# Optimization experiments

Measured on AMD Instinct MI355X. Metric: run time of the kernel, lower is better.

The kernel has to match this reference:

```python
import jax, jax.numpy as jnp
import numpy as np

N = 50000      # nodes
E = 600000     # edges
D_IN = 128
HID = 128
D_OUT = 3
G = 32         # graphs in the batch


def setup_inputs() -> dict:
    key = jax.random.key(0)
    ks = jax.random.split(key, 16)
    s = 0.05
    x = jax.random.normal(ks[0], (N, D_IN), dtype=jnp.float32)
    edge_index = jax.random.randint(ks[1], (2, E), 0, N, dtype=jnp.int64)
    batch = jnp.sort(jax.random.randint(ks[2], (N,), 0, G, dtype=jnp.int64))
    return {
        "x": x,
        "conv0_Wl": jax.random.normal(ks[3], (HID, D_IN), jnp.float32) * s,
        "conv0_bl": jnp.zeros((HID,), jnp.float32),
        "conv0_Wr": jax.random.normal(ks[4], (HID, D_IN), jnp.float32) * s,
        "lin1_W": jax.random.normal(ks[5], (HID, HID), jnp.float32) * s,
        "lin1_b": jnp.zeros((HID,), jnp.float32),
        "conv1_Wl": jax.random.normal(ks[6], (HID, HID), jnp.float32) * s,
        "conv1_bl": jnp.zeros((HID,), jnp.float32),
        "conv1_Wr": jax.random.normal(ks[7], (HID, HID), jnp.float32) * s,
        "fc_W": jax.random.normal(ks[8], (D_OUT, HID), jnp.float32) * s,
        "fc_b": jnp.zeros((D_OUT,), jnp.float32),
        "edge_index": edge_index,
        "batch": batch,
    }


def _sage_conv(x, Wl, bl, Wr, src, dst):
    # PyG SAGEConv (mean aggr): out = lin_l(mean_{j in N(i)} x_j) + lin_r(x_i)
    msg = x[src]                                              # [E, d] gather
    ssum = jax.ops.segment_sum(msg, dst, num_segments=N)      # [N, d]
    cnt = jax.ops.segment_sum(jnp.ones((src.shape[0],), x.dtype), dst, num_segments=N)
    aggr = ssum / jnp.maximum(cnt, 1.0)[:, None]
    return aggr @ Wl.T + bl + x @ Wr.T


def reference(x, conv0_Wl, conv0_bl, conv0_Wr, lin1_W, lin1_b,
              conv1_Wl, conv1_bl, conv1_Wr, fc_W, fc_b,
              edge_index, batch):
    src, dst = edge_index[0], edge_index[1]
    # conv0 -> relu (dropout is identity in eval mode)
    h = jax.nn.relu(_sage_conv(x, conv0_Wl, conv0_bl, conv0_Wr, src, dst))
    # Linear -> relu -> SAGEConv -> relu
    h = jax.nn.relu(h @ lin1_W.T + lin1_b)
    h = jax.nn.relu(_sage_conv(h, conv1_Wl, conv1_bl, conv1_Wr, src, dst))
    # global_mean_pool over graphs
    gsum = jax.ops.segment_sum(h, batch, num_segments=G)
    gcnt = jax.ops.segment_sum(jnp.ones((h.shape[0],), h.dtype), batch, num_segments=G)
    pooled = gsum / jnp.maximum(gcnt, 1.0)[:, None]           # [G, HID]
    return pooled @ fc_W.T + fc_b                             # [G, D_OUT]
```

## Files before the change

kernel.cpp:

```cpp
#include <hip/hip_runtime.h>
#include <hip/hip_bf16.h>
#include <stdint.h>


typedef __attribute__((ext_vector_type(8))) short short8;
typedef __attribute__((ext_vector_type(4))) float f32x4;
typedef __attribute__((ext_vector_type(2))) float f32x2;

__device__ __forceinline__ float bits2f(uint32_t b) {
    union { uint32_t u; float f; } c; c.u = b; return c.f;
}
__device__ __forceinline__ unsigned short f2bf(float f) {
    __hip_bfloat16 h = __float2bfloat16(f);
    union { __hip_bfloat16 h; unsigned short u; } c; c.h = h; return c.u;
}
__device__ __forceinline__ uint32_t pack2bf(float a, float b) {
    return (uint32_t)f2bf(a) | ((uint32_t)f2bf(b) << 16);
}
__device__ __forceinline__ uint32_t pk4fp8(float f0, float f1, float f2, float f3) {
    int o = 0;
    o = __builtin_amdgcn_cvt_pk_fp8_f32(f0, f1, o, false);
    o = __builtin_amdgcn_cvt_pk_fp8_f32(f2, f3, o, true);
    return (uint32_t)o;
}
__device__ __forceinline__ void acc8f8(float* a, uint2 v) {
    f32x2 p0 = __builtin_amdgcn_cvt_pk_f32_fp8((int)v.x, false);
    f32x2 p1 = __builtin_amdgcn_cvt_pk_f32_fp8((int)v.x, true);
    f32x2 p2 = __builtin_amdgcn_cvt_pk_f32_fp8((int)v.y, false);
    f32x2 p3 = __builtin_amdgcn_cvt_pk_f32_fp8((int)v.y, true);
    a[0] += p0.x; a[1] += p0.y; a[2] += p1.x; a[3] += p1.y;
    a[4] += p2.x; a[5] += p2.y; a[6] += p3.x; a[7] += p3.y;
}

__device__ __forceinline__ void detect_flags(const unsigned short* x,
                                             const int* ei,
                                             int& isbf, int& is64) {
    int lane = threadIdx.x & 63;
    unsigned short h = x[lane];
    int e = (h >> 7) & 0xFF;
    unsigned long long mbf = __ballot(e >= 102 && e <= 137);
    unsigned long long m64 = __ballot(ei[2 * lane + 1] != 0);
    isbf = (__popcll(mbf) >= 52) ? 1 : 0;
    is64 = (m64 == 0ULL) ? 1 : 0;
}

#define WB_W0L 0
#define WB_W0R 16384
#define WB_W1  32768
#define WB_W1L 49152
#define WB_W1R 65536
#define WB_TOTAL 81920
#define CF_B0L 0
#define CF_B1  128
#define CF_B1L 256
#define CF_FCW 384
#define CF_FCB 768
#define CF_TOTAL 771

__global__ __launch_bounds__(256) void prep_kernel(
    const void* x, const int* __restrict__ ei,
    const void* s0, const void* s1, const void* s2, const void* s3,
    const void* s4, const void* f0, const void* f1, const void* f2,
    const void* f3, const void* f4,
    unsigned short* __restrict__ Hb, uint2* __restrict__ Xf8,
    unsigned short* __restrict__ wb,
    float* __restrict__ cf, int* __restrict__ cnt, int* __restrict__ nbr,
    int* __restrict__ flags, int n8, int E, int EG, int WC) {
    int isbf, is64;
    detect_flags((const unsigned short*)x, ei, isbf, is64);
    int b = blockIdx.x;
    if (b == 0 && threadIdx.x == 0) { flags[0] = isbf; flags[1] = is64; }

    if (b < EG) {
        int e = b * 256 + threadIdx.x;
        if (e >= E) return;
        int s, d;
        if (is64) { s = ei[2 * e]; d = ei[2 * (E + e)]; }
        else      { s = ei[e];     d = ei[E + e]; }
        int pos = atomicAdd(&cnt[d], 1);
        if (pos < 64) nbr[((size_t)d << 6) + pos] = s;
    } else if (b < EG + WC) {
        int i = (b - EG) * 256 + threadIdx.x;
        if (i < WB_TOTAL) {
            const void* p; int k = i & 16383;
            switch (i >> 14) {
                case 0: p = s0; break;
                case 1: p = s1; break;
                case 2: p = s2; break;
                case 3: p = s3; break;
                default: p = s4; break;
            }
            wb[i] = isbf ? ((const unsigned short*)p)[k]
                         : f2bf(((const float*)p)[k]);
        } else {
            int j = i - WB_TOTAL;
            if (j >= CF_TOTAL) return;
            const void* p; int k;
            if      (j < CF_B1)  { p = f0; k = j; }
            else if (j < CF_B1L) { p = f1; k = j - CF_B1; }
            else if (j < CF_FCW) { p = f2; k = j - CF_B1L; }
            else if (j < CF_FCB) { p = f3; k = j - CF_FCW; }
            else                 { p = f4; k = j - CF_FCB; }
            cf[j] = isbf ? bits2f((uint32_t)((const unsigned short*)p)[k] << 16)
                         : ((const float*)p)[k];
        }
    } else {
        int i = (b - EG - WC) * 256 + threadIdx.x;
        if (i >= n8) return;
        float f[8];
        if (isbf) {
            uint4 d = ((const uint4*)x)[i];
            f[0] = bits2f(d.x << 16); f[1] = bits2f(d.x & 0xffff0000u);
            f[2] = bits2f(d.y << 16); f[3] = bits2f(d.y & 0xffff0000u);
            f[4] = bits2f(d.z << 16); f[5] = bits2f(d.z & 0xffff0000u);
            f[6] = bits2f(d.w << 16); f[7] = bits2f(d.w & 0xffff0000u);
        } else {
            float4 a = ((const float4*)x)[2 * i];
            float4 c = ((const float4*)x)[2 * i + 1];
            f[0] = a.x; f[1] = a.y; f[2] = a.z; f[3] = a.w;
            f[4] = c.x; f[5] = c.y; f[6] = c.z; f[7] = c.w;
            uint4 d;
            d.x = pack2bf(f[0], f[1]); d.y = pack2bf(f[2], f[3]);
            d.z = pack2bf(f[4], f[5]); d.w = pack2bf(f[6], f[7]);
            ((uint4*)Hb)[i] = d;
        }
        uint2 o8;
        o8.x = pk4fp8(f[0], f[1], f[2], f[3]);
        o8.y = pk4fp8(f[4], f[5], f[6], f[7]);
        Xf8[i] = o8;
    }
}

template <bool LIN1, bool POOL>
__device__ __forceinline__ void conv_core(
    const void* xsel, const unsigned short* __restrict__ Hbuf,
    const uint2* __restrict__ G8,
    const int* __restrict__ cnt, const int* __restrict__ nbr,
    const unsigned short* __restrict__ Wl, const unsigned short* __restrict__ Wr,
    const float* __restrict__ bias,
    const unsigned short* __restrict__ W2, const float* __restrict__ bias2,
    unsigned short* __restrict__ Hdst, uint2* __restrict__ Hdst8,
    float* __restrict__ pool, const int* __restrict__ batch,
    const int* __restrict__ flags, int N) {
    __shared__ unsigned short bufA[16 * 136];
    __shared__ unsigned short bufB[LIN1 ? 16 * 136 : 1];
    __shared__ float pbuf[POOL ? 512 : 1];
    const int t = threadIdx.x;
    const int lane = t & 63;
    const int w = t >> 6;
    const int l15 = lane & 15;
    const int kq = lane >> 4;
    const int m0 = blockIdx.x * 16;

    const int flags0 = flags[0];
    const unsigned short* Hs = flags0 ? (const unsigned short*)xsel : Hbuf;

    int f64 = 0, gmin = 0, g[4];
    if (POOL) {
        f64 = flags[1];
        gmin = f64 ? batch[2 * m0] : batch[m0];
#pragma unroll
        for (int r = 0; r < 4; r++) {
            int gr = m0 + kq * 4 + r;
            g[r] = (gr < N) ? (f64 ? batch[2 * gr] : batch[gr]) : -1;
        }
        for (int i = t; i < 512; i += 256) pbuf[i] = 0.f;
    }

    short8 xf[4];
    {
        int xr = m0 + l15; if (xr >= N) xr = N - 1;
        const unsigned short* xrow = Hs + (size_t)xr * 128 + kq * 8;
#pragma unroll
        for (int kc = 0; kc < 4; kc++) xf[kc] = *(const short8*)(xrow + kc * 32);
    }
    float bc[2];
    const int nt0 = w * 2;
    bc[0] = bias[nt0 * 16 + l15];
    bc[1] = bias[(nt0 + 1) * 16 + l15];

    {
        const int row = w * 4 + kq;
        const int node = m0 + row;
        float a[8] = {0.f, 0.f, 0.f, 0.f, 0.f, 0.f, 0.f, 0.f};
        float invd = 0.f;
        if (node < N) {
            int dcnt = cnt[node];
            invd = 1.f / fmaxf((float)dcnt, 1.f);
            if (dcnt > 64) dcnt = 64;
            const int* nrow = nbr + ((size_t)node << 6);
            for (int base = 0; base < dcnt; base += 16) {
                int c = dcnt - base; if (c > 16) c = 16;
                int idx = (l15 < c) ? nrow[base + l15] : 0;
                int it = 0;
                for (; it + 4 <= c; it += 4) {
                    int j0 = __shfl(idx, kq * 16 + it, 64);
                    int j1 = __shfl(idx, kq * 16 + it + 1, 64);
                    int j2 = __shfl(idx, kq * 16 + it + 2, 64);
                    int j3 = __shfl(idx, kq * 16 + it + 3, 64);
                    uint2 v0 = G8[(size_t)j0 * 16 + l15];
                    uint2 v1 = G8[(size_t)j1 * 16 + l15];
                    uint2 v2 = G8[(size_t)j2 * 16 + l15];
                    uint2 v3 = G8[(size_t)j3 * 16 + l15];
                    acc8f8(a, v0); acc8f8(a, v1); acc8f8(a, v2); acc8f8(a, v3);
                }
                for (; it < c; ++it) {
                    int j = __shfl(idx, kq * 16 + it, 64);
                    acc8f8(a, G8[(size_t)j * 16 + l15]);
                }
            }
        }
        uint4 o;
        o.x = pack2bf(a[0] * invd, a[1] * invd);
        o.y = pack2bf(a[2] * invd, a[3] * invd);
        o.z = pack2bf(a[4] * invd, a[5] * invd);
        o.w = pack2bf(a[6] * invd, a[7] * invd);
        *(uint4*)(bufA + row * 136 + l15 * 8) = o;
    }
    __syncthreads();

    short8 af[4];
#pragma unroll
    for (int kc = 0; kc < 4; kc++)
        af[kc] = *(const short8*)(bufA + l15 * 136 + kc * 32 + kq * 8);

    f32x4 acc[2];
    acc[0] = (f32x4){0.f, 0.f, 0.f, 0.f};
    acc[1] = (f32x4){0.f, 0.f, 0.f, 0.f};
#pragma unroll
    for (int kc = 0; kc < 4; kc++) {
#pragma unroll
        for (int u = 0; u < 2; u++) {
            const size_t woff = (size_t)((nt0 + u) * 16 + l15) * 128 + kc * 32 + kq * 8;
            acc[u] = __builtin_amdgcn_mfma_f32_16x16x32_bf16(
                xf[kc], *(const short8*)(Wr + woff), acc[u], 0, 0, 0);
            acc[u] = __builtin_amdgcn_mfma_f32_16x16x32_bf16(
                af[kc], *(const short8*)(Wl + woff), acc[u], 0, 0, 0);
        }
    }

    if (LIN1) {
#pragma unroll
        for (int u = 0; u < 2; u++) {
#pragma unroll
            for (int r = 0; r < 4; r++) {
                bufB[(kq * 4 + r) * 136 + (nt0 + u) * 16 + l15] =
                    f2bf(fmaxf(acc[u][r] + bc[u], 0.f));
            }
        }
        __syncthreads();
        short8 hf[4];
#pragma unroll
        for (int kc = 0; kc < 4; kc++)
            hf[kc] = *(const short8*)(bufB + l15 * 136 + kc * 32 + kq * 8);
        acc[0] = (f32x4){0.f, 0.f, 0.f, 0.f};
        acc[1] = (f32x4){0.f, 0.f, 0.f, 0.f};
        bc[0] = bias2[nt0 * 16 + l15];
        bc[1] = bias2[(nt0 + 1) * 16 + l15];
#pragma unroll
        for (int kc = 0; kc < 4; kc++) {
#pragma unroll
            for (int u = 0; u < 2; u++) {
                const size_t woff = (size_t)((nt0 + u) * 16 + l15) * 128 + kc * 32 + kq * 8;
                acc[u] = __builtin_amdgcn_mfma_f32_16x16x32_bf16(
                    hf[kc], *(const short8*)(W2 + woff), acc[u], 0, 0, 0);
            }
        }
    }

    if (POOL) {
        bool same = (g[0] == g[1]) && (g[1] == g[2]) && (g[2] == g[3]) && (g[0] >= 0);
#pragma unroll
        for (int u = 0; u < 2; u++) {
            int c = (nt0 + u) * 16 + l15;
            float v0 = fmaxf(acc[u][0] + bc[u], 0.f);
            float v1 = fmaxf(acc[u][1] + bc[u], 0.f);
            float v2 = fmaxf(acc[u][2] + bc[u], 0.f);
            float v3 = fmaxf(acc[u][3] + bc[u], 0.f);
            if (same) {
                int si = g[0] - gmin;
                float s4 = (v0 + v1) + (v2 + v3);
                if (si < 4) atomicAdd(&pbuf[si * 128 + c], s4);
                else        atomicAdd(&pool[g[0] * 128 + c], s4);
            } else {
                float vr[4] = {v0, v1, v2, v3};
#pragma unroll
                for (int r = 0; r < 4; r++) {
                    if (g[r] >= 0) {
                        int si = g[r] - gmin;
                        if (si < 4) atomicAdd(&pbuf[si * 128 + c], vr[r]);
                        else        atomicAdd(&pool[g[r] * 128 + c], vr[r]);
                    }
                }
            }
        }
        __syncthreads();
        for (int i = t; i < 512; i += 256) {
            float v = pbuf[i];
            if (v != 0.f)
                atomicAdd(&pool[(gmin + (i >> 7)) * 128 + (i & 127)], v);
        }
    } else {
#pragma unroll
        for (int u = 0; u < 2; u++) {
#pragma unroll
            for (int r = 0; r < 4; r++) {
                bufA[(kq * 4 + r) * 136 + (nt0 + u) * 16 + l15] =
                    f2bf(fmaxf(acc[u][r] + bc[u], 0.f));
            }
        }
        __syncthreads();
        int row = t >> 4, colsh = (t & 15) * 8;
        uint4 val = *(const uint4*)(bufA + row * 136 + colsh);
        if (m0 + row < N) {
            *(uint4*)(Hdst + (size_t)(m0 + row) * 128 + colsh) = val;
            float h0 = bits2f(val.x << 16), h1 = bits2f(val.x & 0xffff0000u);
            float h2 = bits2f(val.y << 16), h3 = bits2f(val.y & 0xffff0000u);
            float h4 = bits2f(val.z << 16), h5 = bits2f(val.z & 0xffff0000u);
            float h6 = bits2f(val.w << 16), h7 = bits2f(val.w & 0xffff0000u);
            uint2 e8;
            e8.x = pk4fp8(h0, h1, h2, h3);
            e8.y = pk4fp8(h4, h5, h6, h7);
            Hdst8[(size_t)(m0 + row) * 16 + (colsh >> 3)] = e8;
        }
    }
}

__global__ __launch_bounds__(256) void conv01_kernel(
    const void* xsel, const unsigned short* __restrict__ Hbuf,
    const uint2* __restrict__ G8,
    const int* __restrict__ cnt, const int* __restrict__ nbr,
    const unsigned short* __restrict__ Wl, const unsigned short* __restrict__ Wr,
    const float* __restrict__ bias,
    const unsigned short* __restrict__ W2, const float* __restrict__ bias2,
    unsigned short* __restrict__ Hdst, uint2* __restrict__ Hdst8,
    const int* __restrict__ flags, int N) {
    conv_core<true, false>(xsel, Hbuf, G8, cnt, nbr, Wl, Wr, bias, W2, bias2,
                           Hdst, Hdst8, nullptr, nullptr, flags, N);
}

__global__ __launch_bounds__(256) void conv1p_kernel(
    const unsigned short* __restrict__ Hbuf, const uint2* __restrict__ G8,
    const int* __restrict__ cnt, const int* __restrict__ nbr,
    const unsigned short* __restrict__ Wl, const unsigned short* __restrict__ Wr,
    const float* __restrict__ bias,
    float* __restrict__ pool, const int* __restrict__ batch,
    const int* __restrict__ flags, int N) {
    conv_core<false, true>(Hbuf, Hbuf, G8, cnt, nbr, Wl, Wr, bias,
                           nullptr, nullptr, nullptr, nullptr, pool, batch,
                           flags, N);
}

__global__ void fc_kernel(const float* __restrict__ pool,
                          const int* __restrict__ batch,
                          const float* __restrict__ W,
                          const float* __restrict__ b,
                          void* __restrict__ out,
                          const int* __restrict__ flags, int N, int G) {
    __shared__ int gst[64];
    int t = threadIdx.x;
    int f64 = flags[1];
    int isbf = flags[0];
    if (t <= G) {
        int lo = 0, hi = N;
        while (lo < hi) {
            int mid = (lo + hi) >> 1;
            int bv = f64 ? batch[2 * mid] : batch[mid];
            if (bv < t) lo = mid + 1; else hi = mid;
        }
        gst[t] = lo;
    }
    __syncthreads();
    if (t >= G * 3) return;
    int g = t / 3, o = t % 3;
    int cnt = gst[g + 1] - gst[g];
    float inv = 1.f / fmaxf((float)cnt, 1.f);
    float acc = 0.f;
    for (int k = 0; k < 128; k++)
        acc += pool[g * 128 + k] * W[o * 128 + k];
    float r = acc * inv + b[o];
    if (isbf) ((__hip_bfloat16*)out)[t] = __float2bfloat16(r);
    else      ((float*)out)[t] = r;
}

extern "C" void kernel_launch(void* const* d_in, const int* in_sizes, int n_in,
                              void* d_out, int out_size, void* d_ws, size_t ws_size,
                              hipStream_t stream) {
    const void* x   = d_in[0];
    const void* W0l = d_in[1];
    const void* b0l = d_in[2];
    const void* W0r = d_in[3];
    const void* W1  = d_in[4];
    const void* b1  = d_in[5];
    const void* W1l = d_in[6];
    const void* b1l = d_in[7];
    const void* W1r = d_in[8];
    const void* fcW = d_in[9];
    const void* fcb = d_in[10];
    const int* edge_index = (const int*)d_in[11];
    const int* batch      = (const int*)d_in[12];

    const int N = in_sizes[12];
    const int E = in_sizes[11] / 2;
    const int G = out_size / 3;

    char* ws = (char*)d_ws;
    auto align64 = [](size_t v) { return (v + 63) & ~(size_t)63; };
    size_t off = 0;
    size_t OFF_CNT  = off; off = align64(off + (size_t)N * 4);
    size_t OFF_POOL = off; off = align64(off + (size_t)G * 128 * 4);
    size_t MEMSET_BYTES = off;
    size_t OFF_FLAGS = off; off = align64(off + 64);
    size_t OFF_NBR  = off; off = align64(off + (size_t)N * 64 * 4);
    size_t OFF_WB   = off; off = align64(off + (size_t)WB_TOTAL * 2);
    size_t OFF_CF   = off; off = align64(off + (size_t)CF_TOTAL * 4);
    size_t OFF_XF8  = off; off = align64(off + (size_t)N * 128);
    size_t OFF_H2F8 = off; off = align64(off + (size_t)N * 128);
    size_t OFF_HB   = off; off = align64(off + ((size_t)N + 64) * 128 * 2);
    size_t OFF_H2   = off; off = align64(off + ((size_t)N + 64) * 128 * 2);
    (void)ws_size;

    int*    cnt    = (int*)(ws + OFF_CNT);
    float*  pool   = (float*)(ws + OFF_POOL);
    int*    flags  = (int*)(ws + OFF_FLAGS);
    int*    nbr    = (int*)(ws + OFF_NBR);
    unsigned short* wb = (unsigned short*)(ws + OFF_WB);
    float*  cf     = (float*)(ws + OFF_CF);
    uint2*  Xf8    = (uint2*)(ws + OFF_XF8);
    uint2*  H2f8   = (uint2*)(ws + OFF_H2F8);
    unsigned short* Hb = (unsigned short*)(ws + OFF_HB);
    unsigned short* H2 = (unsigned short*)(ws + OFF_H2);

    hipMemsetAsync(ws, 0, MEMSET_BYTES, stream);

    int n8 = (N * 128) / 8;
    int EG  = (E + 255) / 256;
    int WC  = (WB_TOTAL + CF_TOTAL + 255) / 256;
    int CVT = (n8 + 255) / 256;
    prep_kernel<<<EG + WC + CVT, 256, 0, stream>>>(
        x, edge_index, W0l, W0r, W1, W1l, W1r, b0l, b1, b1l, fcW, fcb,
        Hb, Xf8, wb, cf, cnt, nbr, flags, n8, E, EG, WC);

    int cgrid = (N + 15) / 16;

    conv01_kernel<<<cgrid, 256, 0, stream>>>(
        x, Hb, Xf8, cnt, nbr, wb + WB_W0L, wb + WB_W0R, cf + CF_B0L,
        wb + WB_W1, cf + CF_B1, H2, H2f8, flags, N);

    conv1p_kernel<<<cgrid, 256, 0, stream>>>(
        H2, H2f8, cnt, nbr, wb + WB_W1L, wb + WB_W1R, cf + CF_B1L,
        pool, batch, flags, N);

    fc_kernel<<<1, 128, 0, stream>>>(pool, batch, cf + CF_FCW, cf + CF_FCB,
                                     d_out, flags, N, G);

    (void)in_sizes; (void)n_in; (void)out_size;
}
```

Baseline: 240.9 us.

## Use persistent blocks with atomic tile counter and batched neighbor gathers

Turns the two conv kernels into persistent kernels capped at 2048 blocks that pull 16-row tiles from a global atomic counter. The next tile index is prefetched into shared memory with double buffering. The first 32 neighbor indices are preloaded and gathered in unrolled chunks of eight loads to raise memory-level parallelism. This is meant to cut block launch overhead and gather latency, at the cost of an extra atomic and barrier per tile and wasted zero-padded loads for low-degree nodes.

```diff
diff --git a/kernel.cpp b/kernel.cpp
--- a/kernel.cpp
+++ b/kernel.cpp
@@ -141,188 +141,234 @@
     const unsigned short* __restrict__ W2, const float* __restrict__ bias2,
     unsigned short* __restrict__ Hdst, uint2* __restrict__ Hdst8,
     float* __restrict__ pool, const int* __restrict__ batch,
-    const int* __restrict__ flags, int N) {
+    const int* __restrict__ flags, int* ctr, int N) {
     __shared__ unsigned short bufA[16 * 136];
     __shared__ unsigned short bufB[LIN1 ? 16 * 136 : 1];
     __shared__ float pbuf[POOL ? 512 : 1];
+    __shared__ int s_next[2];
     const int t = threadIdx.x;
     const int lane = t & 63;
     const int w = t >> 6;
     const int l15 = lane & 15;
     const int kq = lane >> 4;
-    const int m0 = blockIdx.x * 16;
+    const int nt0 = w * 2;
+    const int ntiles = (N + 15) >> 4;
 
     const int flags0 = flags[0];
     const unsigned short* Hs = flags0 ? (const unsigned short*)xsel : Hbuf;
-
-    int f64 = 0, gmin = 0, g[4];
-    if (POOL) {
-        f64 = flags[1];
-        gmin = f64 ? batch[2 * m0] : batch[m0];
-#pragma unroll
-        for (int r = 0; r < 4; r++) {
-            int gr = m0 + kq * 4 + r;
-            g[r] = (gr < N) ? (f64 ? batch[2 * gr] : batch[gr]) : -1;
-        }
-        for (int i = t; i < 512; i += 256) pbuf[i] = 0.f;
+    const int f64 = POOL ? flags[1] : 0;
+
+    const float b0a = bias[nt0 * 16 + l15];
+    const float b0b = bias[(nt0 + 1) * 16 + l15];
+    float b2a = 0.f, b2b = 0.f;
+    if (LIN1) {
+        b2a = bias2[nt0 * 16 + l15];
+        b2b = bias2[(nt0 + 1) * 16 + l15];
     }
 
-    short8 xf[4];
-    {
-        int xr = m0 + l15; if (xr >= N) xr = N - 1;
-        const unsigned short* xrow = Hs + (size_t)xr * 128 + kq * 8;
-#pragma unroll
-        for (int kc = 0; kc < 4; kc++) xf[kc] = *(const short8*)(xrow + kc * 32);
-    }
-    float bc[2];
-    const int nt0 = w * 2;
-    bc[0] = bias[nt0 * 16 + l15];
-    bc[1] = bias[(nt0 + 1) * 16 + l15];
-
-    {
+    if (t == 0) s_next[0] = atomicAdd(ctr, 1);
+    __syncthreads();
+    int tile = s_next[0];
+    int par = 1;
+
+    while (tile < ntiles) {
+        if (t == 0) s_next[par] = atomicAdd(ctr, 1);
+        const int m0 = tile * 16;
+
+        int gmin = 0, g[4];
+        if (POOL) {
+            gmin = f64 ? batch[2 * m0] : batch[m0];
+#pragma unroll
+            for (int r = 0; r < 4; r++) {
+                int gr = m0 + kq * 4 + r;
+                g[r] = (gr < N) ? (f64 ? batch[2 * gr] : batch[gr]) : -1;
+            }
+            for (int i = t; i < 512; i += 256) pbuf[i] = 0.f;
+        }
+
         const int row = w * 4 + kq;
         const int node = m0 + row;
-        float a[8] = {0.f, 0.f, 0.f, 0.f, 0.f, 0.f, 0.f, 0.f};
+        int c = 0;
         float invd = 0.f;
+        const int* nrow = nbr;
+        int i0 = 0, i1 = 0;
         if (node < N) {
             int dcnt = cnt[node];
             invd = 1.f / fmaxf((float)dcnt, 1.f);
-            if (dcnt > 64) dcnt = 64;
-            const int* nrow = nbr + ((size_t)node << 6);
-            for (int base = 0; base < dcnt; base += 16) {
-                int c = dcnt - base; if (c > 16) c = 16;
-                int idx = (l15 < c) ? nrow[base + l15] : 0;
+            c = dcnt > 64 ? 64 : dcnt;
+            nrow = nbr + ((size_t)node << 6);
+            i0 = (l15 < c) ? nrow[l15] : 0;
+            i1 = (16 + l15 < c) ? nrow[16 + l15] : 0;
+        }
+
+        short8 xf[4];
+        {
+            int xr = m0 + l15; if (xr >= N) xr = N - 1;
+            const unsigned short* xrow = Hs + (size_t)xr * 128 + kq * 8;
+#pragma unroll
+            for (int kc = 0; kc < 4; kc++) xf[kc] = *(const short8*)(xrow + kc * 32);
+        }
+
+        {
+            float a[8] = {0.f, 0.f, 0.f, 0.f, 0.f, 0.f, 0.f, 0.f};
+            int nch = (c + 7) >> 3; if (nch > 4) nch = 4;
+#pragma unroll
+            for (int ch = 0; ch < 4; ++ch) {
+                if (ch < nch) {
+                    uint2 vv[8];
+#pragma unroll
+                    for (int u = 0; u < 8; ++u) {
+                        const int s = ch * 8 + u;
+                        int jv = __shfl((s < 16) ? i0 : i1, kq * 16 + (s & 15), 64);
+                        int j = (s < c) ? jv : 0;
+                        vv[u] = G8[(size_t)j * 16 + l15];
+                        if (s >= c) { vv[u].x = 0u; vv[u].y = 0u; }
+                    }
+#pragma unroll
+                    for (int u = 0; u < 8; ++u) acc8f8(a, vv[u]);
+                }
+            }
+            for (int base = 32; base < c; base += 16) {
+                int cc = c - base; if (cc > 16) cc = 16;
+                int idx2 = (l15 < cc) ? nrow[base + l15] : 0;
                 int it = 0;
-                for (; it + 4 <= c; it += 4) {
-                    int j0 = __shfl(idx, kq * 16 + it, 64);
-                    int j1 = __shfl(idx, kq * 16 + it + 1, 64);
-                    int j2 = __shfl(idx, kq * 16 + it + 2, 64);
-                    int j3 = __shfl(idx, kq * 16 + it + 3, 64);
+                for (; it + 4 <= cc; it += 4) {
+                    int j0 = __shfl(idx2, kq * 16 + it, 64);
+                    int j1 = __shfl(idx2, kq * 16 + it + 1, 64);
+                    int j2 = __shfl(idx2, kq * 16 + it + 2, 64);
+                    int j3 = __shfl(idx2, kq * 16 + it + 3, 64);
                     uint2 v0 = G8[(size_t)j0 * 16 + l15];
                     uint2 v1 = G8[(size_t)j1 * 16 + l15];
                     uint2 v2 = G8[(size_t)j2 * 16 + l15];
                     uint2 v3 = G8[(size_t)j3 * 16 + l15];
                     acc8f8(a, v0); acc8f8(a, v1); acc8f8(a, v2); acc8f8(a, v3);
                 }
-                for (; it < c; ++it) {
-                    int j = __shfl(idx, kq * 16 + it, 64);
+                for (; it < cc; ++it) {
+                    int j = __shfl(idx2, kq * 16 + it, 64);
                     acc8f8(a, G8[(size_t)j * 16 + l15]);
                 }
             }
-        }
-        uint4 o;
-        o.x = pack2bf(a[0] * invd, a[1] * invd);
-        o.y = pack2bf(a[2] * invd, a[3] * invd);
-        o.z = pack2bf(a[4] * invd, a[5] * invd);
-        o.w = pack2bf(a[6] * invd, a[7] * invd);
-        *(uint4*)(bufA + row * 136 + l15 * 8) = o;
-    }
-    __syncthreads();
-
-    short8 af[4];
-#pragma unroll
-    for (int kc = 0; kc < 4; kc++)
-        af[kc] = *(const short8*)(bufA + l15 * 136 + kc * 32 + kq * 8);
-
-    f32x4 acc[2];
-    acc[0] = (f32x4){0.f, 0.f, 0.f, 0.f};
-    acc[1] = (f32x4){0.f, 0.f, 0.f, 0.f};
-#pragma unroll
-    for (int kc = 0; kc < 4; kc++) {
-#pragma unroll
-        for (int u = 0; u < 2; u++) {
-            const size_t woff = (size_t)((nt0 + u) * 16 + l15) * 128 + kc * 32 + kq * 8;
-            acc[u] = __builtin_amdgcn_mfma_f32_16x16x32_bf16(
-                xf[kc], *(const short8*)(Wr + woff), acc[u], 0, 0, 0);
-            acc[u] = __builtin_amdgcn_mfma_f32_16x16x32_bf16(
-                af[kc], *(const short8*)(Wl + woff), acc[u], 0, 0, 0);
-        }
-    }
-
-    if (LIN1) {
-#pragma unroll
-        for (int u = 0; u < 2; u++) {
-#pragma unroll
-            for (int r = 0; r < 4; r++) {
-                bufB[(kq * 4 + r) * 136 + (nt0 + u) * 16 + l15] =
-                    f2bf(fmaxf(acc[u][r] + bc[u], 0.f));
-            }
+            uint4 o;
+            o.x = pack2bf(a[0] * invd, a[1] * invd);
+            o.y = pack2bf(a[2] * invd, a[3] * invd);
+            o.z = pack2bf(a[4] * invd, a[5] * invd);
+            o.w = pack2bf(a[6] * invd, a[7] * invd);
+            *(uint4*)(bufA + row * 136 + l15 * 8) = o;
         }
         __syncthreads();
-        short8 hf[4];
+
+        short8 af[4];
 #pragma unroll
         for (int kc = 0; kc < 4; kc++)
-            hf[kc] = *(const short8*)(bufB + l15 * 136 + kc * 32 + kq * 8);
+            af[kc] = *(const short8*)(bufA + l15 * 136 + kc * 32 + kq * 8);
+
+        f32x4 acc[2];
         acc[0] = (f32x4){0.f, 0.f, 0.f, 0.f};
         acc[1] = (f32x4){0.f, 0.f, 0.f, 0.f};
-        bc[0] = bias2[nt0 * 16 + l15];
-        bc[1] = bias2[(nt0 + 1) * 16 + l15];
 #pragma unroll
         for (int kc = 0; kc < 4; kc++) {
 #pragma unroll
             for (int u = 0; u < 2; u++) {
                 const size_t woff = (size_t)((nt0 + u) * 16 + l15) * 128 + kc * 32 + kq * 8;
                 acc[u] = __builtin_amdgcn_mfma_f32_16x16x32_bf16(
-                    hf[kc], *(const short8*)(W2 + woff), acc[u], 0, 0, 0);
-            }
-        }
-    }
-
-    if (POOL) {
-        bool same = (g[0] == g[1]) && (g[1] == g[2]) && (g[2] == g[3]) && (g[0] >= 0);
-#pragma unroll
-        for (int u = 0; u < 2; u++) {
-            int c = (nt0 + u) * 16 + l15;
-            float v0 = fmaxf(acc[u][0] + bc[u], 0.f);
-            float v1 = fmaxf(acc[u][1] + bc[u], 0.f);
-            float v2 = fmaxf(acc[u][2] + bc[u], 0.f);
-            float v3 = fmaxf(acc[u][3] + bc[u], 0.f);
-            if (same) {
-                int si = g[0] - gmin;
-                float s4 = (v0 + v1) + (v2 + v3);
-                if (si < 4) atomicAdd(&pbuf[si * 128 + c], s4);
-                else        atomicAdd(&pool[g[0] * 128 + c], s4);
-            } else {
-                float vr[4] = {v0, v1, v2, v3};
+                    xf[kc], *(const short8*)(Wr + woff), acc[u], 0, 0, 0);
+                acc[u] = __builtin_amdgcn_mfma_f32_16x16x32_bf16(
+                    af[kc], *(const short8*)(Wl + woff), acc[u], 0, 0, 0);
+            }
+        }
+
+        if (LIN1) {
+#pragma unroll
+            for (int u = 0; u < 2; u++) {
+                const float bb = u ? b0b : b0a;
 #pragma unroll
                 for (int r = 0; r < 4; r++) {
-                    if (g[r] >= 0) {
-                        int si = g[r] - gmin;
-                        if (si < 4) atomicAdd(&pbuf[si * 128 + c], vr[r]);
-                        else        atomicAdd(&pool[g[r] * 128 + c], vr[r]);
+                    bufB[(kq * 4 + r) * 136 + (nt0 + u) * 16 + l15] =
+                        f2bf(fmaxf(acc[u][r] + bb, 0.f));
+                }
+            }
+            __syncthreads();
+            short8 hf[4];
+#pragma unroll
+            for (int kc = 0; kc < 4; kc++)
+                hf[kc] = *(const short8*)(bufB + l15 * 136 + kc * 32 + kq * 8);
+            acc[0] = (f32x4){0.f, 0.f, 0.f, 0.f};
+            acc[1] = (f32x4){0.f, 0.f, 0.f, 0.f};
+#pragma unroll
+            for (int kc = 0; kc < 4; kc++) {
+#pragma unroll
+                for (int u = 0; u < 2; u++) {
+                    const size_t woff = (size_t)((nt0 + u) * 16 + l15) * 128 + kc * 32 + kq * 8;
+                    acc[u] = __builtin_amdgcn_mfma_f32_16x16x32_bf16(
+                        hf[kc], *(const short8*)(W2 + woff), acc[u], 0, 0, 0);
+                }
+            }
+        }
+
+        const float ba = LIN1 ? b2a : b0a;
+        const float bb = LIN1 ? b2b : b0b;
+
+        if (POOL) {
+            bool same = (g[0] == g[1]) && (g[1] == g[2]) && (g[2] == g[3]) && (g[0] >= 0);
+#pragma unroll
+            for (int u = 0; u < 2; u++) {
+                int cc = (nt0 + u) * 16 + l15;
+                const float bu = u ? bb : ba;
+                float v0 = fmaxf(acc[u][0] + bu, 0.f);
+                float v1 = fmaxf(acc[u][1] + bu, 0.f);
+                float v2 = fmaxf(acc[u][2] + bu, 0.f);
+                float v3 = fmaxf(acc[u][3] + bu, 0.f);
+                if (same) {
+                    int si = g[0] - gmin;
+                    float s4 = (v0 + v1) + (v2 + v3);
+                    if (si < 4) atomicAdd(&pbuf[si * 128 + cc], s4);
+                    else        atomicAdd(&pool[g[0] * 128 + cc], s4);
+                } else {
+                    float vr[4] = {v0, v1, v2, v3};
+#pragma unroll
+                    for (int r = 0; r < 4; r++) {
+                        if (g[r] >= 0) {
+                            int si = g[r] - gmin;
+                            if (si < 4) atomicAdd(&pbuf[si * 128 + cc], vr[r]);
+                            else        atomicAdd(&pool[g[r] * 128 + cc], vr[r]);
+                        }
                     }
                 }
             }
+            __syncthreads();
+            for (int i = t; i < 512; i += 256) {
+                float v = pbuf[i];
+                if (v != 0.f)
+                    atomicAdd(&pool[(gmin + (i >> 7)) * 128 + (i & 127)], v);
+            }
+        } else {
+#pragma unroll
+            for (int u = 0; u < 2; u++) {
+                const float bu = u ? bb : ba;
+#pragma unroll
+                for (int r = 0; r < 4; r++) {
+                    bufA[(kq * 4 + r) * 136 + (nt0 + u) * 16 + l15] =
+                        f2bf(fmaxf(acc[u][r] + bu, 0.f));
+                }
+            }
+            __syncthreads();
+            int srow = t >> 4, colsh = (t & 15) * 8;
+            uint4 val = *(const uint4*)(bufA + srow * 136 + colsh);
+            if (m0 + srow < N) {
+                *(uint4*)(Hdst + (size_t)(m0 + srow) * 128 + colsh) = val;
+                float h0 = bits2f(val.x << 16), h1 = bits2f(val.x & 0xffff0000u);
+                float h2 = bits2f(val.y << 16), h3 = bits2f(val.y & 0xffff0000u);
+                float h4 = bits2f(val.z << 16), h5 = bits2f(val.z & 0xffff0000u);
+                float h6 = bits2f(val.w << 16), h7 = bits2f(val.w & 0xffff0000u);
+                uint2 e8;
+                e8.x = pk4fp8(h0, h1, h2, h3);
+                e8.y = pk4fp8(h4, h5, h6, h7);
+                Hdst8[(size_t)(m0 + srow) * 16 + (colsh >> 3)] = e8;
+            }
         }
         __syncthreads();
-        for (int i = t; i < 512; i += 256) {
-            float v = pbuf[i];
-            if (v != 0.f)
-                atomicAdd(&pool[(gmin + (i >> 7)) * 128 + (i & 127)], v);
-        }
-    } else {
-#pragma unroll
-        for (int u = 0; u < 2; u++) {
-#pragma unroll
-            for (int r = 0; r < 4; r++) {
-                bufA[(kq * 4 + r) * 136 + (nt0 + u) * 16 + l15] =
-                    f2bf(fmaxf(acc[u][r] + bc[u], 0.f));
-            }
-        }
-        __syncthreads();
-        int row = t >> 4, colsh = (t & 15) * 8;
-        uint4 val = *(const uint4*)(bufA + row * 136 + colsh);
-        if (m0 + row < N) {
-            *(uint4*)(Hdst + (size_t)(m0 + row) * 128 + colsh) = val;
-            float h0 = bits2f(val.x << 16), h1 = bits2f(val.x & 0xffff0000u);
-            float h2 = bits2f(val.y << 16), h3 = bits2f(val.y & 0xffff0000u);
-            float h4 = bits2f(val.z << 16), h5 = bits2f(val.z & 0xffff0000u);
-            float h6 = bits2f(val.w << 16), h7 = bits2f(val.w & 0xffff0000u);
-            uint2 e8;
-            e8.x = pk4fp8(h0, h1, h2, h3);
-            e8.y = pk4fp8(h4, h5, h6, h7);
-            Hdst8[(size_t)(m0 + row) * 16 + (colsh >> 3)] = e8;
-        }
+        tile = s_next[par];
+        par ^= 1;
     }
 }
 
@@ -334,9 +380,9 @@
     const float* __restrict__ bias,
     const unsigned short* __restrict__ W2, const float* __restrict__ bias2,
     unsigned short* __restrict__ Hdst, uint2* __restrict__ Hdst8,
-    const int* __restrict__ flags, int N) {
+    const int* __restrict__ flags, int* ctr, int N) {
     conv_core<true, false>(xsel, Hbuf, G8, cnt, nbr, Wl, Wr, bias, W2, bias2,
-                           Hdst, Hdst8, nullptr, nullptr, flags, N);
+                           Hdst, Hdst8, nullptr, nullptr, flags, ctr, N);
 }
 
 __global__ __launch_bounds__(256) void conv1p_kernel(
@@ -345,10 +391,10 @@
     const unsigned short* __restrict__ Wl, const unsigned short* __restrict__ Wr,
     const float* __restrict__ bias,
     float* __restrict__ pool, const int* __restrict__ batch,
-    const int* __restrict__ flags, int N) {
+    const int* __restrict__ flags, int* ctr, int N) {
     conv_core<false, true>(Hbuf, Hbuf, G8, cnt, nbr, Wl, Wr, bias,
                            nullptr, nullptr, nullptr, nullptr, pool, batch,
-                           flags, N);
+                           flags, ctr, N);
 }
 
 __global__ void fc_kernel(const float* __restrict__ pool,
@@ -409,6 +455,7 @@
     size_t off = 0;
     size_t OFF_CNT  = off; off = align64(off + (size_t)N * 4);
     size_t OFF_POOL = off; off = align64(off + (size_t)G * 128 * 4);
+    size_t OFF_CTR  = off; off = align64(off + 128);
     size_t MEMSET_BYTES = off;
     size_t OFF_FLAGS = off; off = align64(off + 64);
     size_t OFF_NBR  = off; off = align64(off + (size_t)N * 64 * 4);
@@ -422,6 +469,7 @@
 
     int*    cnt    = (int*)(ws + OFF_CNT);
     float*  pool   = (float*)(ws + OFF_POOL);
+    int*    ctr    = (int*)(ws + OFF_CTR);
     int*    flags  = (int*)(ws + OFF_FLAGS);
     int*    nbr    = (int*)(ws + OFF_NBR);
     unsigned short* wb = (unsigned short*)(ws + OFF_WB);
@@ -442,14 +490,15 @@
         Hb, Xf8, wb, cf, cnt, nbr, flags, n8, E, EG, WC);
 
     int cgrid = (N + 15) / 16;
-
-    conv01_kernel<<<cgrid, 256, 0, stream>>>(
+    int pgrid = cgrid < 2048 ? cgrid : 2048;
+
+    conv01_kernel<<<pgrid, 256, 0, stream>>>(
         x, Hb, Xf8, cnt, nbr, wb + WB_W0L, wb + WB_W0R, cf + CF_B0L,
-        wb + WB_W1, cf + CF_B1, H2, H2f8, flags, N);
-
-    conv1p_kernel<<<cgrid, 256, 0, stream>>>(
+        wb + WB_W1, cf + CF_B1, H2, H2f8, flags, ctr, N);
+
+    conv1p_kernel<<<pgrid, 256, 0, stream>>>(
         H2, H2f8, cnt, nbr, wb + WB_W1L, wb + WB_W1R, cf + CF_B1L,
-        pool, batch, flags, N);
+        pool, batch, flags, ctr + 16, N);
 
     fc_kernel<<<1, 128, 0, stream>>>(pool, batch, cf + CF_FCW, cf + CF_FCB,
                                      d_out, flags, N, G);
```

Measured after the change: 264.5 us. 1.1x slower.
